# Optimization experiments

Hardware: AMD Instinct MI355X
Metric: run time of the kernel (lower is better)

Reference implementation:

```python
import jax, jax.numpy as jnp
import numpy as np

B, F, NN, T, H, C = 4096, 32, 8, 100, 512, 8
D = F * NN                      # population-encoded input dim
TAU = 20.0
BETA = float(np.exp(-1.0 / TAU))  # membrane decay per dt=1
THR = 1.0
TW = 1.0 / NN                   # tuning width


def setup_inputs() -> dict:
    key = jax.random.key(0)
    k1, k2, k3, k4 = jax.random.split(key, 4)
    spectral_indices = jax.random.uniform(k1, (B, F), dtype=jnp.float32)
    W1 = jax.random.normal(k2, (H, D), dtype=jnp.float32) / np.sqrt(D)
    W2 = jax.random.normal(k3, (C, H), dtype=jnp.float32) / np.sqrt(H)
    # pre-drawn uniform noise for the Bernoulli population encoder (B,T,D)
    enc_noise = jax.random.uniform(k4, (B, T, D), dtype=jnp.float32)
    return {"spectral_indices": spectral_indices, "W1": W1, "W2": W2,
            "enc_noise": enc_noise}


def reference(spectral_indices, W1, W2, enc_noise):
    # ---- population encoding (TemporalEncoder.population_encode) ----
    preferred = jnp.linspace(0.0, 1.0, NN, dtype=jnp.float32)      # (NN,)
    dist2 = (spectral_indices[..., None] - preferred) ** 2         # (B,F,NN)
    act = jnp.exp(-dist2 / (2.0 * TW * TW)).reshape(B, D)          # (B,D)
    # spikes_t = (rand < act*0.1) at every timestep
    spike_train = (enc_noise < (act * 0.1)[:, None, :]).astype(jnp.float32)  # (B,T,D)

    # ---- 2-layer LIF SNN unrolled via scan ----
    xs = jnp.swapaxes(spike_train, 0, 1)  # (T,B,D)

    def step(carry, x_t):
        m1, m2, acc = carry
        m1 = BETA * m1 + x_t @ W1.T                 # (B,H)
        s1 = (m1 > THR).astype(m1.dtype)
        m1 = m1 * (1.0 - s1)                        # reset to zero on spike
        m2 = BETA * m2 + s1 @ W2.T                  # (B,C)
        s2 = (m2 > THR).astype(m2.dtype)
        m2 = m2 * (1.0 - s2)
        return (m1, m2, acc + s2), None

    init = (jnp.zeros((B, H), jnp.float32),
            jnp.zeros((B, C), jnp.float32),
            jnp.zeros((B, C), jnp.float32))
    (_, _, acc), _ = jax.lax.scan(step, init, xs)
    return acc / T   # output firing rates (B, C)
```

## Files before the change

kernel.cpp:

```cpp
#include <hip/hip_runtime.h>
#include <math.h>

#define B_ 4096
#define F_ 32
#define T_ 100
#define H_ 512
#define C_ 8
#define D_ 256

static __device__ __constant__ float BETA_F = 0.95122942450071400910f;

__global__ void snn_prep(const float* __restrict__ W1,
                         const float* __restrict__ W2,
                         float* __restrict__ ws) {
    float* W1T = ws;
    float* W2T = ws + (size_t)D_ * H_;
    const int bid = blockIdx.x;
    const int tid = threadIdx.x;
    if (bid < D_) {
        const int d = bid;
        W1T[(size_t)d * H_ + tid]       = W1[(size_t)tid * D_ + d];
        W1T[(size_t)d * H_ + tid + 256] = W1[(size_t)(tid + 256) * D_ + d];
    } else {
        for (int h = tid; h < H_; h += 256) {
#pragma unroll
            for (int c = 0; c < C_; ++c)
                W2T[h * C_ + c] = W2[c * H_ + h];
        }
    }
}

__global__ __launch_bounds__(64)
void snn_main(const float* __restrict__ spec,
              const float* __restrict__ ws,
              const float* __restrict__ noise,
              float* __restrict__ out) {
    const int b = blockIdx.x;
    const int lane = threadIdx.x;

    __shared__ unsigned long long s1mask[T_][8];
    __shared__ float u_lds[T_][C_];

    const float* __restrict__ W1T = ws;
    const float* __restrict__ W2T = ws + (size_t)D_ * H_;
    const float* __restrict__ NZb = noise + (size_t)b * T_ * D_;

    float pr[4];
#pragma unroll
    for (int i = 0; i < 4; ++i) {
        const int d = lane + 64 * i;
        const int f = d >> 3, n = d & 7;
        const float s = spec[b * F_ + f];
        const float p = (float)((double)n / 7.0);
        const float diff = s - p;
        const float arg = -32.0f * (diff * diff);
        pr[i] = (float)exp((double)arg) * 0.1f;
    }

    float m1[8];
#pragma unroll
    for (int i = 0; i < 8; ++i) m1[i] = 0.f;

    float nz0 = NZb[lane], nz1 = NZb[64 + lane], nz2 = NZb[128 + lane], nz3 = NZb[192 + lane];

    for (int t = 0; t < T_; ++t) {
        const int tn = (t + 1 < T_) ? (t + 1) : t;
        const float* np_ = NZb + (size_t)tn * D_;
        const float nn0 = np_[lane], nn1 = np_[64 + lane], nn2 = np_[128 + lane], nn3 = np_[192 + lane];

        unsigned long long bm0 = __ballot(nz0 < pr[0]);
        unsigned long long bm1 = __ballot(nz1 < pr[1]);
        unsigned long long bm2 = __ballot(nz2 < pr[2]);
        unsigned long long bm3 = __ballot(nz3 < pr[3]);
        nz0 = nn0; nz1 = nn1; nz2 = nn2; nz3 = nn3;

        float z[8];
#pragma unroll
        for (int i = 0; i < 8; ++i) z[i] = 0.f;

        auto POP = [&]() -> int {
            if (bm0) { const int k = __builtin_ctzll(bm0); bm0 &= bm0 - 1; return k; }
            if (bm1) { const int k = __builtin_ctzll(bm1); bm1 &= bm1 - 1; return 64 + k; }
            if (bm2) { const int k = __builtin_ctzll(bm2); bm2 &= bm2 - 1; return 128 + k; }
            if (bm3) { const int k = __builtin_ctzll(bm3); bm3 &= bm3 - 1; return 192 + k; }
            return -1;
        };

        int da = POP();
        if (da >= 0) {
            const float* ra = W1T + (size_t)da * H_ + lane;
            float wa[8];
#pragma unroll
            for (int i = 0; i < 8; ++i) wa[i] = ra[64 * i];
            int db = POP();
            while (db >= 0) {
                const float* rb = W1T + (size_t)db * H_ + lane;
                float wb[8];
#pragma unroll
                for (int i = 0; i < 8; ++i) wb[i] = rb[64 * i];
#pragma unroll
                for (int i = 0; i < 8; ++i) z[i] += wa[i];
#pragma unroll
                for (int i = 0; i < 8; ++i) wa[i] = wb[i];
                db = POP();
            }
#pragma unroll
            for (int i = 0; i < 8; ++i) z[i] += wa[i];
        }

        unsigned long long sb[8];
#pragma unroll
        for (int i = 0; i < 8; ++i) {
            const float mm = __fadd_rn(__fmul_rn(BETA_F, m1[i]), z[i]);
            const bool s = mm > 1.0f;
            sb[i] = __ballot(s);
            m1[i] = s ? 0.f : mm;
        }
        if (lane == 0) {
#pragma unroll
            for (int i = 0; i < 8; ++i) s1mask[t][i] = sb[i];
        }
    }

    __syncthreads();

#pragma unroll
    for (int rep = 0; rep < 2; ++rep) {
        const int t = lane + rep * 64;
        if (t < T_) {
            unsigned long long sm[8];
#pragma unroll
            for (int j = 0; j < 8; ++j) sm[j] = s1mask[t][j];
            float u[8];
#pragma unroll
            for (int c = 0; c < 8; ++c) u[c] = 0.f;
#pragma unroll
            for (int j = 0; j < 8; ++j) {
                unsigned long long m = sm[j];
                while (m) {
                    const int k = __builtin_ctzll(m);
                    m &= m - 1;
                    const int h = 64 * j + k;
                    const float4 wlo = ((const float4*)(W2T + h * 8))[0];
                    const float4 whi = ((const float4*)(W2T + h * 8))[1];
                    u[0] += wlo.x; u[1] += wlo.y; u[2] += wlo.z; u[3] += wlo.w;
                    u[4] += whi.x; u[5] += whi.y; u[6] += whi.z; u[7] += whi.w;
                }
            }
#pragma unroll
            for (int c = 0; c < 8; ++c) u_lds[t][c] = u[c];
        }
    }

    __syncthreads();

    if (lane < 8) {
        float m2 = 0.f, acc = 0.f;
        for (int t = 0; t < T_; ++t) {
            const float uu = u_lds[t][lane];
            float mm = __fadd_rn(__fmul_rn(BETA_F, m2), uu);
            if (mm > 1.0f) { acc += 1.f; mm = 0.f; }
            m2 = mm;
        }
        out[b * C_ + lane] = acc / 100.0f;
    }
}

extern "C" void kernel_launch(void* const* d_in, const int* in_sizes, int n_in,
                              void* d_out, int out_size, void* d_ws, size_t ws_size,
                              hipStream_t stream) {
    const float* spec  = (const float*)d_in[0];
    const float* W1    = (const float*)d_in[1];
    const float* W2    = (const float*)d_in[2];
    const float* noise = (const float*)d_in[3];
    float* out = (float*)d_out;
    float* ws  = (float*)d_ws;

    snn_prep<<<dim3(D_ + 1), dim3(256), 0, stream>>>(W1, W2, ws);
    snn_main<<<dim3(B_), dim3(64), 0, stream>>>(spec, ws, noise, out);
}
```

Before: 808.1 us.

## Split hidden units across two waves per sample and tile the W1 transpose

The main kernel now runs two wavefronts per batch row, each owning 256 of the 512 hidden neurons. Each lane therefore keeps 4 membrane values instead of 8, and the per-timestep sparse gather of W1 rows is halved per wave and double-buffered explicitly. The prep kernel transposes W1 with a padded shared-memory tile instead of strided global reads. The cost is that both waves redundantly compute the noise ballots and encoding, and the shared-memory layouts change to match the per-wave writes.

```diff
diff --git a/kernel.cpp b/kernel.cpp
--- a/kernel.cpp
+++ b/kernel.cpp
@@ -10,36 +10,50 @@
 
 static __device__ __constant__ float BETA_F = 0.95122942450071400910f;
 
-__global__ void snn_prep(const float* __restrict__ W1,
-                         const float* __restrict__ W2,
-                         float* __restrict__ ws) {
+__global__ __launch_bounds__(256)
+void snn_prep(const float* __restrict__ W1,
+              const float* __restrict__ W2,
+              float* __restrict__ ws) {
     float* W1T = ws;
     float* W2T = ws + (size_t)D_ * H_;
     const int bid = blockIdx.x;
     const int tid = threadIdx.x;
-    if (bid < D_) {
-        const int d = bid;
-        W1T[(size_t)d * H_ + tid]       = W1[(size_t)tid * D_ + d];
-        W1T[(size_t)d * H_ + tid + 256] = W1[(size_t)(tid + 256) * D_ + d];
+    if (bid < 32) {
+        __shared__ float tile[64][65];
+        const int bd = bid & 3;
+        const int bh = bid >> 2;
+        const int tx = tid & 63, ty = tid >> 6;
+#pragma unroll
+        for (int k = 0; k < 16; ++k) {
+            const int r = ty + 4 * k;
+            tile[r][tx] = W1[(size_t)(bh * 64 + r) * D_ + bd * 64 + tx];
+        }
+        __syncthreads();
+#pragma unroll
+        for (int k = 0; k < 16; ++k) {
+            const int r = ty + 4 * k;
+            W1T[(size_t)(bd * 64 + r) * H_ + bh * 64 + tx] = tile[tx][r];
+        }
     } else {
-        for (int h = tid; h < H_; h += 256) {
-#pragma unroll
-            for (int c = 0; c < C_; ++c)
-                W2T[h * C_ + c] = W2[c * H_ + h];
+        for (int i = tid; i < C_ * H_; i += 256) {
+            const int c = i >> 9, h = i & 511;
+            W2T[h * C_ + c] = W2[i];
         }
     }
 }
 
-__global__ __launch_bounds__(64)
+__global__ __launch_bounds__(128, 8)
 void snn_main(const float* __restrict__ spec,
               const float* __restrict__ ws,
               const float* __restrict__ noise,
               float* __restrict__ out) {
     const int b = blockIdx.x;
-    const int lane = threadIdx.x;
-
-    __shared__ unsigned long long s1mask[T_][8];
-    __shared__ float u_lds[T_][C_];
+    const int tid = threadIdx.x;
+    const int lane = tid & 63;
+    const int w = tid >> 6;
+
+    __shared__ unsigned long long s1mask[8][T_];
+    __shared__ float u_lds[C_][T_];
 
     const float* __restrict__ W1T = ws;
     const float* __restrict__ W2T = ws + (size_t)D_ * H_;
@@ -47,21 +61,23 @@
 
     float pr[4];
 #pragma unroll
-    for (int i = 0; i < 4; ++i) {
-        const int d = lane + 64 * i;
+    for (int j = 0; j < 4; ++j) {
+        const int d = lane + 64 * j;
         const int f = d >> 3, n = d & 7;
         const float s = spec[b * F_ + f];
         const float p = (float)((double)n / 7.0);
         const float diff = s - p;
         const float arg = -32.0f * (diff * diff);
-        pr[i] = (float)exp((double)arg) * 0.1f;
-    }
-
-    float m1[8];
-#pragma unroll
-    for (int i = 0; i < 8; ++i) m1[i] = 0.f;
+        pr[j] = (float)exp((double)arg) * 0.1f;
+    }
+
+    float m1[4];
+#pragma unroll
+    for (int i = 0; i < 4; ++i) m1[i] = 0.f;
 
     float nz0 = NZb[lane], nz1 = NZb[64 + lane], nz2 = NZb[128 + lane], nz3 = NZb[192 + lane];
+
+    const float* __restrict__ W1Tw = W1T + 256 * w + lane;
 
     for (int t = 0; t < T_; ++t) {
         const int tn = (t + 1 < T_) ? (t + 1) : t;
@@ -74,9 +90,9 @@
         unsigned long long bm3 = __ballot(nz3 < pr[3]);
         nz0 = nn0; nz1 = nn1; nz2 = nn2; nz3 = nn3;
 
-        float z[8];
-#pragma unroll
-        for (int i = 0; i < 8; ++i) z[i] = 0.f;
+        float z[4];
+#pragma unroll
+        for (int i = 0; i < 4; ++i) z[i] = 0.f;
 
         auto POP = [&]() -> int {
             if (bm0) { const int k = __builtin_ctzll(bm0); bm0 &= bm0 - 1; return k; }
@@ -86,83 +102,91 @@
             return -1;
         };
 
-        int da = POP();
-        if (da >= 0) {
-            const float* ra = W1T + (size_t)da * H_ + lane;
-            float wa[8];
-#pragma unroll
-            for (int i = 0; i < 8; ++i) wa[i] = ra[64 * i];
-            int db = POP();
-            while (db >= 0) {
-                const float* rb = W1T + (size_t)db * H_ + lane;
-                float wb[8];
-#pragma unroll
-                for (int i = 0; i < 8; ++i) wb[i] = rb[64 * i];
-#pragma unroll
-                for (int i = 0; i < 8; ++i) z[i] += wa[i];
-#pragma unroll
-                for (int i = 0; i < 8; ++i) wa[i] = wb[i];
-                db = POP();
+        {
+            int d0 = POP();
+            if (d0 >= 0) {
+                float A[4], B[4];
+                {
+                    const float* r = W1Tw + (size_t)d0 * H_;
+#pragma unroll
+                    for (int i = 0; i < 4; ++i) A[i] = r[64 * i];
+                }
+                for (;;) {
+                    int d1 = POP();
+                    if (d1 < 0) {
+#pragma unroll
+                        for (int i = 0; i < 4; ++i) z[i] += A[i];
+                        break;
+                    }
+                    {
+                        const float* r = W1Tw + (size_t)d1 * H_;
+#pragma unroll
+                        for (int i = 0; i < 4; ++i) B[i] = r[64 * i];
+                    }
+#pragma unroll
+                    for (int i = 0; i < 4; ++i) z[i] += A[i];
+                    d0 = POP();
+                    if (d0 < 0) {
+#pragma unroll
+                        for (int i = 0; i < 4; ++i) z[i] += B[i];
+                        break;
+                    }
+                    {
+                        const float* r = W1Tw + (size_t)d0 * H_;
+#pragma unroll
+                        for (int i = 0; i < 4; ++i) A[i] = r[64 * i];
+                    }
+#pragma unroll
+                    for (int i = 0; i < 4; ++i) z[i] += B[i];
+                }
             }
-#pragma unroll
-            for (int i = 0; i < 8; ++i) z[i] += wa[i];
-        }
-
-        unsigned long long sb[8];
-#pragma unroll
-        for (int i = 0; i < 8; ++i) {
+        }
+
+#pragma unroll
+        for (int i = 0; i < 4; ++i) {
             const float mm = __fadd_rn(__fmul_rn(BETA_F, m1[i]), z[i]);
             const bool s = mm > 1.0f;
-            sb[i] = __ballot(s);
+            const unsigned long long sb = __ballot(s);
             m1[i] = s ? 0.f : mm;
-        }
-        if (lane == 0) {
-#pragma unroll
-            for (int i = 0; i < 8; ++i) s1mask[t][i] = sb[i];
+            if (lane == 0) s1mask[4 * w + i][t] = sb;
         }
     }
 
     __syncthreads();
 
-#pragma unroll
-    for (int rep = 0; rep < 2; ++rep) {
-        const int t = lane + rep * 64;
-        if (t < T_) {
-            unsigned long long sm[8];
-#pragma unroll
-            for (int j = 0; j < 8; ++j) sm[j] = s1mask[t][j];
-            float u[8];
-#pragma unroll
-            for (int c = 0; c < 8; ++c) u[c] = 0.f;
-#pragma unroll
-            for (int j = 0; j < 8; ++j) {
-                unsigned long long m = sm[j];
-                while (m) {
-                    const int k = __builtin_ctzll(m);
-                    m &= m - 1;
-                    const int h = 64 * j + k;
-                    const float4 wlo = ((const float4*)(W2T + h * 8))[0];
-                    const float4 whi = ((const float4*)(W2T + h * 8))[1];
-                    u[0] += wlo.x; u[1] += wlo.y; u[2] += wlo.z; u[3] += wlo.w;
-                    u[4] += whi.x; u[5] += whi.y; u[6] += whi.z; u[7] += whi.w;
-                }
+    if (tid < T_) {
+        const int t = tid;
+        float u[8];
+#pragma unroll
+        for (int c = 0; c < 8; ++c) u[c] = 0.f;
+#pragma unroll
+        for (int j = 0; j < 8; ++j) {
+            unsigned long long m = s1mask[j][t];
+            while (m) {
+                const int k = __builtin_ctzll(m);
+                m &= m - 1;
+                const int h = 64 * j + k;
+                const float4 wlo = ((const float4*)(W2T + h * 8))[0];
+                const float4 whi = ((const float4*)(W2T + h * 8))[1];
+                u[0] += wlo.x; u[1] += wlo.y; u[2] += wlo.z; u[3] += wlo.w;
+                u[4] += whi.x; u[5] += whi.y; u[6] += whi.z; u[7] += whi.w;
             }
-#pragma unroll
-            for (int c = 0; c < 8; ++c) u_lds[t][c] = u[c];
-        }
+        }
+#pragma unroll
+        for (int c = 0; c < 8; ++c) u_lds[c][t] = u[c];
     }
 
     __syncthreads();
 
-    if (lane < 8) {
+    if (tid < 8) {
         float m2 = 0.f, acc = 0.f;
         for (int t = 0; t < T_; ++t) {
-            const float uu = u_lds[t][lane];
+            const float uu = u_lds[tid][t];
             float mm = __fadd_rn(__fmul_rn(BETA_F, m2), uu);
             if (mm > 1.0f) { acc += 1.f; mm = 0.f; }
             m2 = mm;
         }
-        out[b * C_ + lane] = acc / 100.0f;
+        out[b * C_ + tid] = acc / 100.0f;
     }
 }
 
@@ -176,6 +200,6 @@
     float* out = (float*)d_out;
     float* ws  = (float*)d_ws;
 
-    snn_prep<<<dim3(D_ + 1), dim3(256), 0, stream>>>(W1, W2, ws);
-    snn_main<<<dim3(B_), dim3(64), 0, stream>>>(spec, ws, noise, out);
+    snn_prep<<<dim3(33), dim3(256), 0, stream>>>(W1, W2, ws);
+    snn_main<<<dim3(B_), dim3(128), 0, stream>>>(spec, ws, noise, out);
 }
```

Measured after the change: 830.3 us. 2.8% more time.
